# Optimization experiments

Measured on AMD Instinct MI355X. Metric: run time of the kernel, lower is better.

Reference implementation:

```python
import math
import jax, jax.numpy as jnp
import numpy as np

# ---- config (matches init_kwargs) ----
HIDDEN = 2048
N_HEADS = 16
Q_LORA = 1536
KV_LORA = 512
NOPE = 128
ROPE = 64
VHD = 128
QHD = NOPE + ROPE  # 192
BASE = 10000.0
SCALE = 40.0
ORIG_MAX = 4096
BETA_FAST = 32
BETA_SLOW = 1
MSCALE = 1.0
MSCALE_ALL = 1.0
EPS = 1e-6


def yarn_get_mscale(scale=1.0, mscale=1.0):
    if scale <= 1:
        return 1.0
    return 0.1 * mscale * math.log(scale) + 1.0


def yarn_cos_sin(seq_len):
    dim = ROPE
    ar = np.arange(0, dim, 2, dtype=np.float32)
    freq_extra = 1.0 / BASE ** (ar / dim)
    freq_inter = 1.0 / (SCALE * BASE ** (ar / dim))
    low = math.floor(dim * math.log(ORIG_MAX / (BETA_FAST * 2 * math.pi)) / (2 * math.log(BASE)))
    high = math.ceil(dim * math.log(ORIG_MAX / (BETA_SLOW * 2 * math.pi)) / (2 * math.log(BASE)))
    low, high = max(low, 0), min(high, dim - 1)
    denom = (high - low) if high != low else 0.001
    ramp = np.clip((np.arange(dim // 2, dtype=np.float32) - low) / denom, 0.0, 1.0)
    inv_freq_mask = 1.0 - ramp
    inv_freq = freq_inter * (1.0 - inv_freq_mask) + freq_extra * inv_freq_mask
    t = np.arange(seq_len, dtype=np.float32)
    freqs = np.outer(t, inv_freq)
    emb = np.concatenate([freqs, freqs], axis=-1)
    _m = yarn_get_mscale(SCALE, MSCALE) / yarn_get_mscale(SCALE, MSCALE_ALL)
    return jnp.asarray(np.cos(emb) * _m), jnp.asarray(np.sin(emb) * _m)


def rms_norm(x, w, eps=EPS):
    xf = x.astype(jnp.float32)
    var = jnp.mean(xf * xf, axis=-1, keepdims=True)
    return (w * (xf * jax.lax.rsqrt(var + eps)).astype(x.dtype))


def _rotate_half(x):
    x1, x2 = jnp.split(x, 2, axis=-1)
    return jnp.concatenate([-x2, x1], axis=-1)


def _interleave_to_half(x):
    # view(b,h,s,d//2,2).transpose(4,3).reshape(b,h,s,d)
    b, h, s, d = x.shape
    return jnp.swapaxes(x.reshape(b, h, s, d // 2, 2), -1, -2).reshape(b, h, s, d)


def apply_rope(q, k, cos, sin, position_ids):
    cos = cos[position_ids][:, None]  # [b,1,s,d]
    sin = sin[position_ids][:, None]
    q = _interleave_to_half(q)
    k = _interleave_to_half(k)
    q_emb = q * cos + _rotate_half(q) * sin
    k_emb = k * cos + _rotate_half(k) * sin
    return q_emb, k_emb


def mla_forward(hidden_states, position_ids, wq_a, q_a_ln_w, wq_b, wkv_a, kv_a_ln_w, wkv_b, wo):
    b, s, _ = hidden_states.shape
    # Q: low-rank down, RMSNorm, up
    q = rms_norm(hidden_states @ wq_a.T, q_a_ln_w) @ wq_b.T        # [b,s,H*QHD]
    q = q.reshape(b, s, N_HEADS, QHD).transpose(0, 2, 1, 3)        # [b,H,s,QHD]
    q_nope, q_pe = q[..., :NOPE], q[..., NOPE:]
    # KV: compressed latent + shared rope key
    ckv = hidden_states @ wkv_a.T                                   # [b,s,KV_LORA+ROPE]
    compressed, k_pe = ckv[..., :KV_LORA], ckv[..., KV_LORA:]
    k_pe = k_pe.reshape(b, s, 1, ROPE).transpose(0, 2, 1, 3)       # [b,1,s,ROPE]
    kv = rms_norm(compressed, kv_a_ln_w) @ wkv_b.T                  # [b,s,H*(NOPE+VHD)]
    kv = kv.reshape(b, s, N_HEADS, NOPE + VHD).transpose(0, 2, 1, 3)
    k_nope, value_states = kv[..., :NOPE], kv[..., NOPE:]
    # decoupled RoPE on rope dims only
    cos, sin = yarn_cos_sin(s)
    q_pe, k_pe = apply_rope(q_pe, k_pe, cos, sin, position_ids)
    query = jnp.concatenate([q_nope, q_pe], axis=-1)                # [b,H,s,QHD]
    key = jnp.concatenate(
        [k_nope, jnp.broadcast_to(k_pe, (b, N_HEADS, s, ROPE))], axis=-1)
    # softmax scale with YaRN mscale correction
    softmax_scale = QHD ** -0.5
    if MSCALE_ALL:
        m = yarn_get_mscale(SCALE, MSCALE_ALL)
        softmax_scale = softmax_scale * m * m
    attn = jnp.einsum('bhqd,bhkd->bhqk', query, key) * softmax_scale
    causal = jnp.tril(jnp.ones((s, s), dtype=bool))
    attn = jnp.where(causal, attn, jnp.finfo(attn.dtype).min)
    attn = jax.nn.softmax(attn.astype(jnp.float32), axis=-1).astype(query.dtype)
    out = jnp.einsum('bhqk,bhkd->bhqd', attn, value_states)         # [b,H,s,VHD]
    out = out.transpose(0, 2, 1, 3).reshape(b, s, N_HEADS * VHD)
    return out @ wo.T


def setup_inputs() -> dict:
    key = jax.random.key(0)
    ks = jax.random.split(key, 8)
    b, s = 2, 2048
    std = 0.02
    return {
        'hidden_states': jax.random.normal(ks[0], (b, s, HIDDEN), jnp.float32),
        'position_ids': jnp.broadcast_to(jnp.arange(s, dtype=jnp.int32), (b, s)),
        'wq_a': jax.random.normal(ks[1], (Q_LORA, HIDDEN), jnp.float32) * std,
        'q_a_ln_w': jnp.ones((Q_LORA,), jnp.float32),
        'wq_b': jax.random.normal(ks[2], (N_HEADS * QHD, Q_LORA), jnp.float32) * std,
        'wkv_a': jax.random.normal(ks[3], (KV_LORA + ROPE, HIDDEN), jnp.float32) * std,
        'kv_a_ln_w': jnp.ones((KV_LORA,), jnp.float32),
        'wkv_b': jax.random.normal(ks[4], (N_HEADS * (NOPE + VHD), KV_LORA), jnp.float32) * std,
        'wo': jax.random.normal(ks[5], (HIDDEN, N_HEADS * VHD), jnp.float32) * std,
    }


def reference(hidden_states, position_ids, wq_a, q_a_ln_w, wq_b, wkv_a, kv_a_ln_w, wkv_b, wo):
    return mla_forward(hidden_states, position_ids, wq_a, q_a_ln_w, wq_b,
                       wkv_a, kv_a_ln_w, wkv_b, wo)
```

## Files before the change

kernel.cpp:

```cpp
#include <hip/hip_runtime.h>
#include <hip/hip_bf16.h>
#include <math.h>

typedef __bf16 bf16_t;
typedef __bf16 bf16x4 __attribute__((ext_vector_type(4)));
typedef __bf16 bf16x8 __attribute__((ext_vector_type(8)));
typedef float floatx4 __attribute__((ext_vector_type(4)));

#define MFMA16(a, b, c) __builtin_amdgcn_mfma_f32_16x16x32_bf16((a), (b), (c), 0, 0, 0)

#define NEG_BIG (-1e30f)

__device__ __forceinline__ void gload16(const bf16_t* g, bf16_t* l) {
    __builtin_amdgcn_global_load_lds(
        (const __attribute__((address_space(1))) unsigned int*)g,
        (__attribute__((address_space(3))) unsigned int*)l,
        16, 0, 0);
}

__global__ void detect_kernel(const unsigned int* __restrict__ lnw, int* __restrict__ flag) {
    if (threadIdx.x == 0 && blockIdx.x == 0)
        flag[0] = (lnw[0] == 0x3F803F80u) ? 1 : 0;
}

__global__ __launch_bounds__(256) void conv_in_kernel(const void* __restrict__ src,
                                                      bf16_t* __restrict__ dst,
                                                      long nchunk,
                                                      const int* __restrict__ flag) {
    long i = (long)blockIdx.x * 256 + threadIdx.x;
    if (i >= nchunk) return;
    if (flag[0]) {
        ((uint4*)dst)[i] = ((const uint4*)src)[i];
    } else {
        const float* f = (const float*)src + i * 8;
        bf16x8 o;
#pragma unroll
        for (int j = 0; j < 8; ++j) o[j] = (bf16_t)f[j];
        ((bf16x8*)dst)[i] = o;
    }
}

__global__ __launch_bounds__(256) void conv_in_scale_kernel(const void* __restrict__ src,
                                                            bf16_t* __restrict__ dst,
                                                            long nchunk,
                                                            const int* __restrict__ flag,
                                                            float s) {
    long i = (long)blockIdx.x * 256 + threadIdx.x;
    if (i >= nchunk) return;
    bf16x8 o;
    if (flag[0]) {
        bf16x8 v = ((const bf16x8*)src)[i];
#pragma unroll
        for (int j = 0; j < 8; ++j) o[j] = (bf16_t)((float)v[j] * s);
    } else {
        const float* f = (const float*)src + i * 8;
#pragma unroll
        for (int j = 0; j < 8; ++j) o[j] = (bf16_t)(f[j] * s);
    }
    ((bf16x8*)dst)[i] = o;
}

__global__ __launch_bounds__(256) void conv_out_kernel(const bf16_t* __restrict__ src,
                                                       void* __restrict__ dst,
                                                       long nchunk,
                                                       const int* __restrict__ flag) {
    long i = (long)blockIdx.x * 256 + threadIdx.x;
    if (i >= nchunk) return;
    bf16x8 v = ((const bf16x8*)src)[i];
    if (flag[0]) {
        ((uint4*)dst)[i] = *(const uint4*)&v;
    } else {
        float* f = (float*)dst + i * 8;
#pragma unroll
        for (int j = 0; j < 8; ++j) f[j] = (float)v[j];
    }
}

__global__ __launch_bounds__(256) void pad_wkv_kernel(const void* __restrict__ src,
                                                      bf16_t* __restrict__ dst,
                                                      const int* __restrict__ flag) {
    long idx = (long)blockIdx.x * 256 + threadIdx.x;
    long e0 = idx * 8;
    if (e0 >= (long)640 * 2048) return;
    int row = (int)(e0 >> 11);
    bf16x8 v;
#pragma unroll
    for (int j = 0; j < 8; ++j) v[j] = (bf16_t)0.0f;
    if (row < 576) {
        if (flag[0]) {
            v = *(const bf16x8*)((const bf16_t*)src + e0);
        } else {
            const float* f = (const float*)src + e0;
#pragma unroll
            for (int j = 0; j < 8; ++j) v[j] = (bf16_t)f[j];
        }
    }
    *(bf16x8*)(dst + e0) = v;
}

#define GEMM_STAGE(bufsel) do { \
        gload16(Ag, &As[bufsel][(wave * 2 + 0) * 512]); \
        gload16(Ag + r16, &As[bufsel][(wave * 2 + 1) * 512]); \
        gload16(Bg, &Bs[bufsel][(wave * 2 + 0) * 512]); \
        gload16(Bg + r16, &Bs[bufsel][(wave * 2 + 1) * 512]); \
        Ag += 32; Bg += 32; } while (0)

#define GEMM_PIPELINE_BODY \
    int tid = threadIdx.x; \
    int lane = tid & 63; \
    int wave = tid >> 6; \
    int m0 = blockIdx.x * 128; \
    int n0 = blockIdx.y * 128; \
    int wm = (wave & 1) * 64; \
    int wn = (wave >> 1) * 64; \
    int col = lane & 15; \
    int g = lane >> 4; \
    floatx4 acc[4][4] = {}; \
    int srow = wave * 32 + (lane >> 2); \
    int scol = ((lane & 3) ^ (srow & 3)) * 8; \
    const bf16_t* Ag = A + (size_t)(m0 + srow) * K + scol; \
    const bf16_t* Bg = B + (size_t)(n0 + srow) * K + scol; \
    size_t r16 = (size_t)16 * K; \
    int rchunk = (g ^ (col & 3)) * 8; \
    int nk = K >> 5; \
    GEMM_STAGE(0); \
    GEMM_STAGE(1); \
    int cur = 0; \
    for (int kt = 0; kt < nk; ++kt) { \
        if (kt + 1 < nk) asm volatile("s_waitcnt vmcnt(4)" ::: "memory"); \
        else             asm volatile("s_waitcnt vmcnt(0)" ::: "memory"); \
        __builtin_amdgcn_s_barrier(); \
        __builtin_amdgcn_sched_barrier(0); \
        bf16x8 af[4], bfr[4]; \
        _Pragma("unroll") \
        for (int i = 0; i < 4; ++i) af[i] = *(const bf16x8*)(&As[cur][(wm + i * 16 + col) * 32 + rchunk]); \
        _Pragma("unroll") \
        for (int j = 0; j < 4; ++j) bfr[j] = *(const bf16x8*)(&Bs[cur][(wn + j * 16 + col) * 32 + rchunk]); \
        _Pragma("unroll") \
        for (int i = 0; i < 4; ++i) \
            _Pragma("unroll") \
            for (int j = 0; j < 4; ++j) \
                acc[i][j] = MFMA16(af[i], bfr[j], acc[i][j]); \
        __builtin_amdgcn_sched_barrier(0); \
        __builtin_amdgcn_s_barrier(); \
        if (kt + 2 < nk) { GEMM_STAGE(cur); } \
        cur ^= 1; \
    }

__global__ __launch_bounds__(256) void gemm_bf16(const bf16_t* __restrict__ A,
                                                 const bf16_t* __restrict__ B,
                                                 bf16_t* __restrict__ C,
                                                 int M, int N, int K) {
    __shared__ __align__(16) bf16_t As[2][128 * 32];
    __shared__ __align__(16) bf16_t Bs[2][128 * 32];
    GEMM_PIPELINE_BODY

#pragma unroll
    for (int i = 0; i < 4; ++i)
#pragma unroll
        for (int j = 0; j < 4; ++j) {
            size_t mrow = (size_t)(m0 + wm + i * 16 + g * 4);
            size_t ncol = (size_t)(n0 + wn + j * 16 + col);
            bf16_t* cp = C + mrow * N + ncol;
#pragma unroll
            for (int r = 0; r < 4; ++r) cp[(size_t)r * N] = (bf16_t)acc[i][j][r];
        }
}

__global__ __launch_bounds__(256) void gemm_kv(const bf16_t* __restrict__ A,
                                               const bf16_t* __restrict__ B,
                                               bf16_t* __restrict__ kn,
                                               bf16_t* __restrict__ vT,
                                               int K) {
    __shared__ __align__(16) bf16_t As[2][128 * 32];
    __shared__ __align__(16) bf16_t Bs[2][128 * 32];
    GEMM_PIPELINE_BODY

#pragma unroll
    for (int i = 0; i < 4; ++i)
#pragma unroll
        for (int j = 0; j < 4; ++j) {
            int mrow = m0 + wm + i * 16 + g * 4;
            int ncol = n0 + wn + j * 16 + col;
            int h = ncol >> 8;
            int within = ncol & 255;
            if (within < 128) {
#pragma unroll
                for (int r = 0; r < 4; ++r)
                    kn[(size_t)(mrow + r) * 2048 + h * 128 + within] = (bf16_t)acc[i][j][r];
            } else {
                int d = within - 128;
                int bb = mrow >> 11;
                int s = mrow & 2047;
                bf16x4 pk;
#pragma unroll
                for (int r = 0; r < 4; ++r) pk[r] = (bf16_t)acc[i][j][r];
                *(bf16x4*)(vT + ((size_t)(bb * 16 + h) * 128 + d) * 2048 + s) = pk;
            }
        }
}

__global__ __launch_bounds__(256) void rmsnorm_kernel(const bf16_t* __restrict__ in, int in_stride,
                                                      const bf16_t* __restrict__ w,
                                                      bf16_t* __restrict__ out, int out_stride,
                                                      int C) {
    int row = blockIdx.x;
    int tid = threadIdx.x;
    const bf16_t* x = in + (size_t)row * in_stride;
    bool act = tid * 8 < C;
    float xs[8];
    float ss = 0.f;
    if (act) {
        bf16x8 v = *(const bf16x8*)(x + tid * 8);
#pragma unroll
        for (int j = 0; j < 8; ++j) {
            xs[j] = (float)v[j];
            ss += xs[j] * xs[j];
        }
    }
    for (int o = 32; o; o >>= 1) ss += __shfl_xor(ss, o, 64);
    __shared__ float red[4];
    if ((tid & 63) == 0) red[tid >> 6] = ss;
    __syncthreads();
    float tot = red[0] + red[1] + red[2] + red[3];
    float scale = rsqrtf(tot / (float)C + 1e-6f);
    if (act) {
        bf16x8 wv = *(const bf16x8*)(w + tid * 8);
        bf16x8 ov;
#pragma unroll
        for (int j = 0; j < 8; ++j) ov[j] = (bf16_t)((float)wv[j] * xs[j] * scale);
        *(bf16x8*)(out + (size_t)row * out_stride + tid * 8) = ov;
    }
}

__global__ __launch_bounds__(256) void rope_kernel(bf16_t* __restrict__ q,
                                                   bf16_t* __restrict__ ckv,
                                                   const int* __restrict__ pos_ids) {
    int tid = threadIdx.x;
    int lane = tid & 63;
    int gwave = (blockIdx.x * 256 + tid) >> 6;
    int unit = gwave * 2 + ((lane >> 5) & 1);
    int j = lane & 31;
    if (unit >= 4096 * 17) return;
    int t = unit / 17;
    int head = unit % 17;

    float fe = __expf(-(float)j * 0.28782313662425575f);
    float fi = fe * 0.025f;
    float ramp = fminf(fmaxf(((float)j - 10.0f) / 13.0f, 0.0f), 1.0f);
    float invf = fi * ramp + fe * (1.0f - ramp);
    float th = (float)pos_ids[t] * invf;
    float c = cosf(th);
    float s = sinf(th);

    bf16_t* base = (head < 16) ? (q + (size_t)t * 3072 + head * 192 + 128)
                               : (ckv + (size_t)t * 640 + 512);
    float e = (float)base[2 * j];
    float o = (float)base[2 * j + 1];
    base[j] = (bf16_t)(e * c - o * s);
    base[j + 32] = (bf16_t)(o * c + e * s);
}

__global__ __launch_bounds__(512, 4) void attn_kernel(const bf16_t* __restrict__ q,
                                                      const bf16_t* __restrict__ kn,
                                                      const bf16_t* __restrict__ ckv,
                                                      const bf16_t* __restrict__ vT,
                                                      bf16_t* __restrict__ outp) {
    __shared__ __align__(16) bf16_t Ks[64][192];
    __shared__ __align__(16) bf16_t Vt[128][64];
    __shared__ __align__(16) bf16_t Ps[8][16][64];

    int tid = threadIdx.x;
    int lane = tid & 63;
    int wave = tid >> 6;
    int x = blockIdx.x, y = blockIdx.y;
    int qt0 = x >> 1;
    int qt = (x & 1) ? (15 - qt0) : qt0;
    if (y >= 16) qt = 15 - qt;
    int b = y >> 4;
    int h = y & 15;
    int q0 = qt * 128;
    size_t tok0 = (size_t)b * 2048;
    int col = lane & 15;
    int g = lane >> 4;

    bf16x8 qf[6];
    {
        const bf16_t* qb = q + (tok0 + q0 + wave * 16 + col) * 3072 + h * 192 + g * 8;
#pragma unroll
        for (int ks = 0; ks < 6; ++ks)
            qf[ks] = *(const bf16x8*)(qb + ks * 32);
    }

    const bf16_t* kg[3]; int kstep[3]; bf16_t* kl[3];
#pragma unroll
    for (int i = 0; i < 3; ++i) {
        int c = tid + i * 512;
        int row = c / 24;
        int ch = c % 24;
        if (ch < 16) { kg[i] = kn + (tok0 + row) * 2048 + h * 128 + ch * 8; kstep[i] = 64 * 2048; }
        else         { kg[i] = ckv + (tok0 + row) * 640 + 512 + (ch - 16) * 8; kstep[i] = 64 * 640; }
        kl[i] = &Ks[row][(ch ^ (row & 7)) * 8];
    }
    const bf16_t* vg[2]; bf16_t* vl[2];
#pragma unroll
    for (int i = 0; i < 2; ++i) {
        int c = tid + i * 512;
        int d = c >> 3;
        int ch = c & 7;
        vg[i] = vT + ((size_t)y * 128 + d) * 2048 + ch * 8;
        vl[i] = &Vt[d][(ch ^ (d & 7)) * 8];
    }

    float m_i = NEG_BIG;
    float l_i = 0.f;
    floatx4 o_acc[8] = {};

    char* PsW = (char*)&Ps[wave][0][0];
    int xsw = col & 7;

    uint4 kpre[3], vpre[2];
#pragma unroll
    for (int i = 0; i < 3; ++i) { kpre[i] = *(const uint4*)kg[i]; kg[i] += kstep[i]; }
#pragma unroll
    for (int i = 0; i < 2; ++i) { vpre[i] = *(const uint4*)vg[i]; vg[i] += 64; }

    int niter = (q0 + 128) >> 6;
    for (int kt = 0; kt < niter; ++kt) {
        int k0 = kt * 64;

        __syncthreads();
#pragma unroll
        for (int i = 0; i < 3; ++i) *(uint4*)kl[i] = kpre[i];
#pragma unroll
        for (int i = 0; i < 2; ++i) *(uint4*)vl[i] = vpre[i];
        __syncthreads();

        if (kt + 1 < niter) {
#pragma unroll
            for (int i = 0; i < 3; ++i) { kpre[i] = *(const uint4*)kg[i]; kg[i] += kstep[i]; }
#pragma unroll
            for (int i = 0; i < 2; ++i) { vpre[i] = *(const uint4*)vg[i]; vg[i] += 64; }
        }

        if (k0 > q0 + wave * 16 + 15) continue;

        floatx4 s_acc[4] = {};
#pragma unroll
        for (int ks = 0; ks < 6; ++ks) {
            bf16x8 ak[4];
#pragma unroll
            for (int mt = 0; mt < 4; ++mt)
                ak[mt] = *(const bf16x8*)(&Ks[mt * 16 + col][((4 * ks + g) ^ xsw) * 8]);
            __builtin_amdgcn_s_setprio(1);
#pragma unroll
            for (int mt = 0; mt < 4; ++mt)
                s_acc[mt] = MFMA16(ak[mt], qf[ks], s_acc[mt]);
            __builtin_amdgcn_s_setprio(0);
        }

        {
            int qg = q0 + wave * 16 + col;
            float mx = NEG_BIG;
            if (k0 + 63 > q0 + wave * 16) {
#pragma unroll
                for (int mt = 0; mt < 4; ++mt)
#pragma unroll
                    for (int r = 0; r < 4; ++r) {
                        int key = k0 + mt * 16 + g * 4 + r;
                        float s = (key <= qg) ? s_acc[mt][r] : NEG_BIG;
                        s_acc[mt][r] = s;
                        mx = fmaxf(mx, s);
                    }
            } else {
#pragma unroll
                for (int mt = 0; mt < 4; ++mt)
#pragma unroll
                    for (int r = 0; r < 4; ++r) mx = fmaxf(mx, s_acc[mt][r]);
            }
            mx = fmaxf(mx, __shfl_xor(mx, 16, 64));
            mx = fmaxf(mx, __shfl_xor(mx, 32, 64));
            bool defer = __all(mx <= m_i + 8.0f);
            float mnew = defer ? m_i : fmaxf(m_i, mx);
            float rs = 0.f;
#pragma unroll
            for (int mt = 0; mt < 4; ++mt) {
                bf16x4 pk;
#pragma unroll
                for (int r = 0; r < 4; ++r) {
                    float p = __expf(s_acc[mt][r] - mnew);
                    rs += p;
                    pk[r] = (bf16_t)p;
                }
                int boff = (col * 128 + mt * 32 + g * 8) ^ ((col & 7) << 4);
                *(bf16x4*)(PsW + boff) = pk;
            }
            rs += __shfl_xor(rs, 16, 64);
            rs += __shfl_xor(rs, 32, 64);
            if (defer) {
                l_i += rs;
            } else {
                float alpha = __expf(m_i - mnew);
                l_i = l_i * alpha + rs;
                m_i = mnew;
#pragma unroll
                for (int mt = 0; mt < 8; ++mt)
#pragma unroll
                    for (int r = 0; r < 4; ++r)
                        o_acc[mt][r] *= alpha;
            }
        }

        asm volatile("s_waitcnt lgkmcnt(0)" ::: "memory");
        __builtin_amdgcn_sched_barrier(0);

#pragma unroll
        for (int kc = 0; kc < 2; ++kc) {
            bf16x8 bp;
            {
                int boff = (col * 128 + kc * 64 + g * 16) ^ ((col & 7) << 4);
                bp = *(const bf16x8*)(PsW + boff);
            }
#pragma unroll
            for (int mt = 0; mt < 8; ++mt) {
                bf16x8 av = *(const bf16x8*)(&Vt[mt * 16 + col][((4 * kc + g) ^ xsw) * 8]);
                __builtin_amdgcn_s_setprio(1);
                o_acc[mt] = MFMA16(av, bp, o_acc[mt]);
                __builtin_amdgcn_s_setprio(0);
            }
        }
    }

    {
        float inv = 1.0f / l_i;
        size_t trow = tok0 + q0 + wave * 16 + col;
        bf16_t* op = outp + trow * 2048 + h * 128;
#pragma unroll
        for (int mt = 0; mt < 8; ++mt) {
            bf16x4 pk;
#pragma unroll
            for (int r = 0; r < 4; ++r) pk[r] = (bf16_t)(o_acc[mt][r] * inv);
            *(bf16x4*)(op + mt * 16 + g * 4) = pk;
        }
    }
}

extern "C" void kernel_launch(void* const* d_in, const int* in_sizes, int n_in,
                              void* d_out, int out_size, void* d_ws, size_t ws_size,
                              hipStream_t stream) {
    const void* hidden_raw = d_in[0];
    const int* pos = (const int*)d_in[1];
    const void* wq_a_raw = d_in[2];
    const void* q_ln_raw = d_in[3];
    const void* wq_b_raw = d_in[4];
    const void* wkv_a_raw = d_in[5];
    const void* kv_ln_raw = d_in[6];
    const void* wkv_b_raw = d_in[7];
    const void* wo_raw = d_in[8];

    char* ws = (char*)d_ws;
    int* flag = (int*)ws;          ws += 256;
    bf16_t* wkv_pad = (bf16_t*)ws; ws += (size_t)640 * 2048 * 2;
    bf16_t* q_a     = (bf16_t*)ws; ws += (size_t)4096 * 1536 * 2;
    bf16_t* qbuf    = (bf16_t*)ws; ws += (size_t)4096 * 3072 * 2;
    bf16_t* ckv     = (bf16_t*)ws; ws += (size_t)4096 * 640 * 2;
    bf16_t* kv_n    = (bf16_t*)ws; ws += (size_t)4096 * 512 * 2;
    bf16_t* knbuf   = (bf16_t*)ws; ws += (size_t)4096 * 2048 * 2;
    bf16_t* vTbuf   = (bf16_t*)ws; ws += (size_t)4096 * 2048 * 2;
    bf16_t* attno   = (bf16_t*)ws; ws += (size_t)4096 * 2048 * 2;
    bf16_t* outbf   = (bf16_t*)ws; ws += (size_t)4096 * 2048 * 2;
    bf16_t* hb      = (bf16_t*)ws; ws += (size_t)4096 * 2048 * 2;
    bf16_t* wqab    = (bf16_t*)ws; ws += (size_t)1536 * 2048 * 2;
    bf16_t* wqbb    = (bf16_t*)ws; ws += (size_t)3072 * 1536 * 2;
    bf16_t* wkvbb   = (bf16_t*)ws; ws += (size_t)4096 * 512 * 2;
    bf16_t* wob     = (bf16_t*)ws; ws += (size_t)2048 * 2048 * 2;
    bf16_t* qlnb    = (bf16_t*)ws; ws += 4096;
    bf16_t* kvlnb   = (bf16_t*)ws; ws += 4096;

    detect_kernel<<<1, 64, 0, stream>>>((const unsigned int*)q_ln_raw, flag);

    double m = 0.1 * log(40.0) + 1.0;
    float scale = (float)((m * m) / sqrt(192.0));

    conv_in_kernel<<<4096, 256, 0, stream>>>(hidden_raw, hb, (long)4096 * 2048 / 8, flag);
    conv_in_kernel<<<1536, 256, 0, stream>>>(wq_a_raw, wqab, (long)1536 * 2048 / 8, flag);
    conv_in_kernel<<<1, 256, 0, stream>>>(q_ln_raw, qlnb, 1536 / 8, flag);
    conv_in_scale_kernel<<<2304, 256, 0, stream>>>(wq_b_raw, wqbb, (long)3072 * 1536 / 8, flag, scale);
    conv_in_kernel<<<1, 256, 0, stream>>>(kv_ln_raw, kvlnb, 512 / 8, flag);
    conv_in_kernel<<<1024, 256, 0, stream>>>(wkv_b_raw, wkvbb, (long)4096 * 512 / 8, flag);
    conv_in_kernel<<<2048, 256, 0, stream>>>(wo_raw, wob, (long)2048 * 2048 / 8, flag);
    pad_wkv_kernel<<<640, 256, 0, stream>>>(wkv_a_raw, wkv_pad, flag);

    gemm_bf16<<<dim3(32, 12), 256, 0, stream>>>(hb, wqab, q_a, 4096, 1536, 2048);
    gemm_bf16<<<dim3(32, 5), 256, 0, stream>>>(hb, wkv_pad, ckv, 4096, 640, 2048);

    rmsnorm_kernel<<<4096, 256, 0, stream>>>(q_a, 1536, qlnb, q_a, 1536, 1536);
    rmsnorm_kernel<<<4096, 256, 0, stream>>>(ckv, 640, kvlnb, kv_n, 512, 512);

    gemm_bf16<<<dim3(32, 24), 256, 0, stream>>>(q_a, wqbb, qbuf, 4096, 3072, 1536);
    gemm_kv<<<dim3(32, 32), 256, 0, stream>>>(kv_n, wkvbb, knbuf, vTbuf, 512);

    rope_kernel<<<8704, 256, 0, stream>>>(qbuf, ckv, pos);

    attn_kernel<<<dim3(16, 32), 512, 0, stream>>>(qbuf, knbuf, ckv, vTbuf, attno);

    gemm_bf16<<<dim3(32, 16), 256, 0, stream>>>(attno, wob, outbf, 4096, 2048, 2048);

    conv_out_kernel<<<4096, 256, 0, stream>>>(outbf, d_out, (long)4096 * 2048 / 8, flag);
}
```

Baseline: 511.3 us.

## Keep softmax probabilities in registers and permute V layout to match MFMA operands

The P tile no longer goes through shared memory. The V tile is stored in LDS with a permuted key order, so the S accumulator registers can feed the PV MFMA as the B operand directly. The exp is switched to exp2 with log2(e) folded into the query weight scale. V reads are batched ahead of the MFMA group. This removes the LDS round trip and the waitcnt barrier per tile, but V stores become two 8-byte writes, which may raise bank conflicts.

```diff
diff --git a/kernel.cpp b/kernel.cpp
--- a/kernel.cpp
+++ b/kernel.cpp
@@ -268,7 +268,6 @@
                                                       bf16_t* __restrict__ outp) {
     __shared__ __align__(16) bf16_t Ks[64][192];
     __shared__ __align__(16) bf16_t Vt[128][64];
-    __shared__ __align__(16) bf16_t Ps[8][16][64];
 
     int tid = threadIdx.x;
     int lane = tid & 63;
@@ -302,21 +301,23 @@
         else         { kg[i] = ckv + (tok0 + row) * 640 + 512 + (ch - 16) * 8; kstep[i] = 64 * 640; }
         kl[i] = &Ks[row][(ch ^ (row & 7)) * 8];
     }
-    const bf16_t* vg[2]; bf16_t* vl[2];
+    const bf16_t* vg[2]; bf16_t* vl0[2]; bf16_t* vl1[2];
 #pragma unroll
     for (int i = 0; i < 2; ++i) {
         int c = tid + i * 512;
         int d = c >> 3;
         int ch = c & 7;
         vg[i] = vT + ((size_t)y * 128 + d) * 2048 + ch * 8;
-        vl[i] = &Vt[d][(ch ^ (d & 7)) * 8];
+        int s0 = (ch >> 2) * 32 + ((2 * ch) & 3) * 8 + ((ch >> 1) & 1) * 4;
+        int s1 = (ch >> 2) * 32 + ((2 * ch + 1) & 3) * 8 + ((ch >> 1) & 1) * 4;
+        vl0[i] = &Vt[d][(((s0 >> 3) ^ (d & 7)) << 3) + (s0 & 7)];
+        vl1[i] = &Vt[d][(((s1 >> 3) ^ (d & 7)) << 3) + (s1 & 7)];
     }
 
     float m_i = NEG_BIG;
     float l_i = 0.f;
     floatx4 o_acc[8] = {};
 
-    char* PsW = (char*)&Ps[wave][0][0];
     int xsw = col & 7;
 
     uint4 kpre[3], vpre[2];
@@ -333,7 +334,12 @@
 #pragma unroll
         for (int i = 0; i < 3; ++i) *(uint4*)kl[i] = kpre[i];
 #pragma unroll
-        for (int i = 0; i < 2; ++i) *(uint4*)vl[i] = vpre[i];
+        for (int i = 0; i < 2; ++i) {
+            uint2 h0 = make_uint2(vpre[i].x, vpre[i].y);
+            uint2 h1 = make_uint2(vpre[i].z, vpre[i].w);
+            *(uint2*)vl0[i] = h0;
+            *(uint2*)vl1[i] = h1;
+        }
         __syncthreads();
 
         if (kt + 1 < niter) {
@@ -359,6 +365,7 @@
             __builtin_amdgcn_s_setprio(0);
         }
 
+        bf16x8 bp[2];
         {
             int qg = q0 + wave * 16 + col;
             float mx = NEG_BIG;
@@ -384,23 +391,24 @@
             float mnew = defer ? m_i : fmaxf(m_i, mx);
             float rs = 0.f;
 #pragma unroll
-            for (int mt = 0; mt < 4; ++mt) {
-                bf16x4 pk;
-#pragma unroll
-                for (int r = 0; r < 4; ++r) {
-                    float p = __expf(s_acc[mt][r] - mnew);
-                    rs += p;
-                    pk[r] = (bf16_t)p;
-                }
-                int boff = (col * 128 + mt * 32 + g * 8) ^ ((col & 7) << 4);
-                *(bf16x4*)(PsW + boff) = pk;
+            for (int kc = 0; kc < 2; ++kc) {
+                bf16x8 t;
+#pragma unroll
+                for (int half = 0; half < 2; ++half)
+#pragma unroll
+                    for (int r = 0; r < 4; ++r) {
+                        float p = exp2f(s_acc[kc * 2 + half][r] - mnew);
+                        rs += p;
+                        t[half * 4 + r] = (bf16_t)p;
+                    }
+                bp[kc] = t;
             }
             rs += __shfl_xor(rs, 16, 64);
             rs += __shfl_xor(rs, 32, 64);
             if (defer) {
                 l_i += rs;
             } else {
-                float alpha = __expf(m_i - mnew);
+                float alpha = exp2f(m_i - mnew);
                 l_i = l_i * alpha + rs;
                 m_i = mnew;
 #pragma unroll
@@ -411,23 +419,17 @@
             }
         }
 
-        asm volatile("s_waitcnt lgkmcnt(0)" ::: "memory");
-        __builtin_amdgcn_sched_barrier(0);
-
 #pragma unroll
         for (int kc = 0; kc < 2; ++kc) {
-            bf16x8 bp;
-            {
-                int boff = (col * 128 + kc * 64 + g * 16) ^ ((col & 7) << 4);
-                bp = *(const bf16x8*)(PsW + boff);
-            }
-#pragma unroll
-            for (int mt = 0; mt < 8; ++mt) {
-                bf16x8 av = *(const bf16x8*)(&Vt[mt * 16 + col][((4 * kc + g) ^ xsw) * 8]);
-                __builtin_amdgcn_s_setprio(1);
-                o_acc[mt] = MFMA16(av, bp, o_acc[mt]);
-                __builtin_amdgcn_s_setprio(0);
-            }
+            bf16x8 av[8];
+#pragma unroll
+            for (int mt = 0; mt < 8; ++mt)
+                av[mt] = *(const bf16x8*)(&Vt[mt * 16 + col][((4 * kc + g) ^ xsw) * 8]);
+            __builtin_amdgcn_s_setprio(1);
+#pragma unroll
+            for (int mt = 0; mt < 8; ++mt)
+                o_acc[mt] = MFMA16(av[mt], bp[kc], o_acc[mt]);
+            __builtin_amdgcn_s_setprio(0);
         }
     }
 
@@ -480,7 +482,7 @@
     detect_kernel<<<1, 64, 0, stream>>>((const unsigned int*)q_ln_raw, flag);
 
     double m = 0.1 * log(40.0) + 1.0;
-    float scale = (float)((m * m) / sqrt(192.0));
+    float scale = (float)((m * m) / sqrt(192.0) * 1.4426950408889634);
 
     conv_in_kernel<<<4096, 256, 0, stream>>>(hidden_raw, hb, (long)4096 * 2048 / 8, flag);
     conv_in_kernel<<<1536, 256, 0, stream>>>(wq_a_raw, wqab, (long)1536 * 2048 / 8, flag);
```

Result: slower. 536.1 us (+4.9%).
